# Optimization experiments

Hardware: AMD Instinct MI355X
Metric: run time of the kernel (lower is better)

Reference implementation:

```python
import jax, jax.numpy as jnp
import numpy as np

B, T, D = 4, 2048, 1024
N, H = 16, 64          # num_heads, key_dim = D // N
F = 4096               # intermediate_dim
SOFT_CAP = 50.0
EPS = 1e-6


def layer_norm(x, gamma, beta, eps=EPS):
    mean = jnp.mean(x, axis=-1, keepdims=True)
    var = jnp.var(x, axis=-1, keepdims=True)
    return (x - mean) * jax.lax.rsqrt(var + eps) * gamma + beta


def setup_inputs() -> dict:
    key = jax.random.key(0)
    ks = jax.random.split(key, 16)
    s = 0.02
    return {
        "inputs": jax.random.normal(ks[0], (B, T, D), dtype=jnp.float32),
        "ln1_gamma": jnp.ones((D,), jnp.float32),
        "ln1_beta": jnp.zeros((D,), jnp.float32),
        "wq": jax.random.normal(ks[1], (D, N, H), jnp.float32) * s,
        "bq": jnp.zeros((N, H), jnp.float32),
        "wk": jax.random.normal(ks[2], (D, N, H), jnp.float32) * s,
        "bk": jnp.zeros((N, H), jnp.float32),
        "wv": jax.random.normal(ks[3], (D, N, H), jnp.float32) * s,
        "bv": jnp.zeros((N, H), jnp.float32),
        "wo": jax.random.normal(ks[4], (N, H, D), jnp.float32) * s,
        "bo": jnp.zeros((D,), jnp.float32),
        "ln2_gamma": jnp.ones((D,), jnp.float32),
        "ln2_beta": jnp.zeros((D,), jnp.float32),
        "w1": jax.random.normal(ks[5], (D, F), jnp.float32) * s,
        "b1": jax.random.normal(ks[6], (F,), jnp.float32) * 1e-6,
        "w2": jax.random.normal(ks[7], (F, D), jnp.float32) * s,
        "b2": jax.random.normal(ks[8], (D,), jnp.float32) * 1e-6,
    }


def reference(inputs, ln1_gamma, ln1_beta, wq, bq, wk, bk, wv, bv, wo, bo,
              ln2_gamma, ln2_beta, w1, b1, w2, b2):
    # --- pre-norm attention branch ---
    x = layer_norm(inputs, ln1_gamma, ln1_beta)
    q = jnp.einsum('btd,dnh->btnh', x, wq) + bq
    k = jnp.einsum('btd,dnh->btnh', x, wk) + bk
    v = jnp.einsum('btd,dnh->btnh', x, wv) + bv
    q = q * (1.0 / jnp.sqrt(jnp.float32(H)))
    score = jnp.einsum('btnh,bsnh->bnts', q, k)          # [B,N,T,T]
    score = SOFT_CAP * jnp.tanh(score / SOFT_CAP)        # logit soft cap
    weights = jax.nn.softmax(score.astype(jnp.float32), axis=-1).astype(q.dtype)
    context = jnp.einsum('bnts,bsnh->btnh', weights, v)
    attn_out = jnp.einsum('btnh,nhd->btd', context, wo) + bo
    x_res = attn_out + inputs
    # --- pre-norm MLP branch ---
    y = layer_norm(x_res, ln2_gamma, ln2_beta)
    y = jax.nn.gelu(y @ w1 + b1, approximate=False)
    y = y @ w2 + b2
    return x_res + y
```

## Files before the change

### kernel.cpp

```cpp
#include <hip/hip_runtime.h>
#include <hip/hip_bf16.h>
#include <math.h>

typedef __attribute__((ext_vector_type(8))) short short8;
typedef __attribute__((ext_vector_type(4))) short short4v;
typedef __attribute__((ext_vector_type(4))) float f32x4;

#define GAS __attribute__((address_space(1)))
#define LAS __attribute__((address_space(3)))

__device__ __forceinline__ LAS void* to_lds(void* p) {
    return (LAS void*)(unsigned)(uintptr_t)p;
}

constexpr int Bc = 4, Tc = 2048, Dc = 1024, Nheads = 16, Hc = 64, Fc = 4096;
constexpr int Mrows = Bc * Tc;
constexpr float LNEPS = 1e-6f;

__device__ __forceinline__ float gelu_exact(float x) {
    return 0.5f * x * (1.0f + erff(x * 0.70710678118654752440f));
}

__global__ __launch_bounds__(256) void transpose_cvt(const float* __restrict__ src,
                                                     __hip_bfloat16* __restrict__ dst,
                                                     int K, int N) {
    __shared__ float tile[32][33];
    const int n0 = blockIdx.x * 32, k0 = blockIdx.y * 32;
    const int tx = threadIdx.x & 31, ty = threadIdx.x >> 5;
    #pragma unroll
    for (int i = 0; i < 32; i += 8)
        tile[ty + i][tx] = src[(size_t)(k0 + ty + i) * N + (n0 + tx)];
    __syncthreads();
    #pragma unroll
    for (int i = 0; i < 32; i += 8)
        dst[(size_t)(n0 + ty + i) * K + (k0 + tx)] = __float2bfloat16(tile[tx][ty + i]);
}

__global__ void concat_bias(const float* __restrict__ bq, const float* __restrict__ bk,
                            const float* __restrict__ bv, float* __restrict__ dst) {
    int i = blockIdx.x * 256 + threadIdx.x;
    float v = (i < 1024) ? bq[i] : (i < 2048 ? bk[i - 1024] : bv[i - 2048]);
    dst[i] = v;
}

__global__ __launch_bounds__(256) void ln_kernel(const float* __restrict__ x,
                                                 const float* __restrict__ gamma,
                                                 const float* __restrict__ beta,
                                                 __hip_bfloat16* __restrict__ out) {
    __shared__ float2 red[4];
    const int row = blockIdx.x, tid = threadIdx.x;
    const float* xr = x + (size_t)row * Dc;
    float4 v = ((const float4*)xr)[tid];
    float s  = v.x + v.y + v.z + v.w;
    float ss = v.x * v.x + v.y * v.y + v.z * v.z + v.w * v.w;
    #pragma unroll
    for (int o = 32; o; o >>= 1) { s += __shfl_down(s, o, 64); ss += __shfl_down(ss, o, 64); }
    if ((tid & 63) == 0) red[tid >> 6] = make_float2(s, ss);
    __syncthreads();
    float2 r0 = red[0], r1 = red[1], r2 = red[2], r3 = red[3];
    s  = r0.x + r1.x + r2.x + r3.x;
    ss = r0.y + r1.y + r2.y + r3.y;
    const float mean = s * (1.0f / Dc);
    const float var  = ss * (1.0f / Dc) - mean * mean;
    const float inv  = rsqrtf(var + LNEPS);
    float4 g  = ((const float4*)gamma)[tid];
    float4 bb = ((const float4*)beta)[tid];
    __hip_bfloat16* orow = out + (size_t)row * Dc + tid * 4;
    orow[0] = __float2bfloat16((v.x - mean) * inv * g.x + bb.x);
    orow[1] = __float2bfloat16((v.y - mean) * inv * g.y + bb.y);
    orow[2] = __float2bfloat16((v.z - mean) * inv * g.z + bb.z);
    orow[3] = __float2bfloat16((v.w - mean) * inv * g.w + bb.w);
}

template <int EPI, bool OUT_BF16>
__global__ __launch_bounds__(256) void gemm_kernel(
    const __hip_bfloat16* __restrict__ A, const __hip_bfloat16* __restrict__ Bt,
    const float* __restrict__ bias, const float* __restrict__ resid,
    void* __restrict__ Cout, int M, int N, int K) {
    __shared__ __align__(16) short As[128 * 32];
    __shared__ __align__(16) short Bs[128 * 32];
    const int tid = threadIdx.x;
    const int wave = tid >> 6, lane = tid & 63, quad = lane >> 4, l16 = lane & 15;
    const int m0 = blockIdx.x * 128, n0 = blockIdx.y * 128;
    const int wm = (wave >> 1) * 64, wn = (wave & 1) * 64;
    f32x4 acc[4][4] = {};

    const int srow = wave * 16 + (lane >> 2);
    const int scol = (lane & 3) * 8;
    const short* aSrc0 = (const short*)A  + (size_t)(m0 + srow) * K + scol;
    const short* aSrc1 = aSrc0 + (size_t)64 * K;
    const short* bSrc0 = (const short*)Bt + (size_t)(n0 + srow) * K + scol;
    const short* bSrc1 = bSrc0 + (size_t)64 * K;
    LAS void* ldsA0 = to_lds(&As[(wave * 16) * 32]);
    LAS void* ldsA1 = to_lds(&As[(64 + wave * 16) * 32]);
    LAS void* ldsB0 = to_lds(&Bs[(wave * 16) * 32]);
    LAS void* ldsB1 = to_lds(&Bs[(64 + wave * 16) * 32]);

    for (int k0 = 0; k0 < K; k0 += 32) {
        __builtin_amdgcn_global_load_lds((const GAS void*)(aSrc0 + k0), ldsA0, 16, 0, 0);
        __builtin_amdgcn_global_load_lds((const GAS void*)(aSrc1 + k0), ldsA1, 16, 0, 0);
        __builtin_amdgcn_global_load_lds((const GAS void*)(bSrc0 + k0), ldsB0, 16, 0, 0);
        __builtin_amdgcn_global_load_lds((const GAS void*)(bSrc1 + k0), ldsB1, 16, 0, 0);
        __syncthreads();
        short8 af[4], bfr[4];
        #pragma unroll
        for (int i = 0; i < 4; i++) af[i]  = *(const short8*)&As[(wm + i * 16 + l16) * 32 + quad * 8];
        #pragma unroll
        for (int i = 0; i < 4; i++) bfr[i] = *(const short8*)&Bs[(wn + i * 16 + l16) * 32 + quad * 8];
        #pragma unroll
        for (int i = 0; i < 4; i++)
            #pragma unroll
            for (int j = 0; j < 4; j++)
                acc[i][j] = __builtin_amdgcn_mfma_f32_16x16x32_bf16(af[i], bfr[j], acc[i][j], 0, 0, 0);
        __syncthreads();
    }
    #pragma unroll
    for (int i = 0; i < 4; i++) {
        #pragma unroll
        for (int j = 0; j < 4; j++) {
            const int col = n0 + wn + j * 16 + l16;
            const float bv = bias[col];
            #pragma unroll
            for (int r = 0; r < 4; r++) {
                const int row = m0 + wm + i * 16 + quad * 4 + r;
                float val = acc[i][j][r] + bv;
                if (EPI == 1) val = gelu_exact(val);
                if (EPI == 2) val += resid[(size_t)row * N + col];
                if (OUT_BF16)
                    ((__hip_bfloat16*)Cout)[(size_t)row * N + col] = __float2bfloat16(val);
                else
                    ((float*)Cout)[(size_t)row * N + col] = val;
            }
        }
    }
}

__global__ __launch_bounds__(256) void gemm_splitk(
    const __hip_bfloat16* __restrict__ A, const __hip_bfloat16* __restrict__ Bt,
    const float* __restrict__ bias, const float* __restrict__ resid,
    float* __restrict__ out, int M, int N, int K, int Kslice) {
    __shared__ __align__(16) short As[128 * 32];
    __shared__ __align__(16) short Bs[128 * 32];
    const int tid = threadIdx.x;
    const int wave = tid >> 6, lane = tid & 63, quad = lane >> 4, l16 = lane & 15;
    const int m0 = blockIdx.x * 128, n0 = blockIdx.y * 128;
    const int kz = blockIdx.z;
    const int wm = (wave >> 1) * 64, wn = (wave & 1) * 64;
    f32x4 acc[4][4] = {};

    const int srow = wave * 16 + (lane >> 2);
    const int scol = (lane & 3) * 8 + kz * Kslice;
    const short* aSrc0 = (const short*)A  + (size_t)(m0 + srow) * K + scol;
    const short* aSrc1 = aSrc0 + (size_t)64 * K;
    const short* bSrc0 = (const short*)Bt + (size_t)(n0 + srow) * K + scol;
    const short* bSrc1 = bSrc0 + (size_t)64 * K;
    LAS void* ldsA0 = to_lds(&As[(wave * 16) * 32]);
    LAS void* ldsA1 = to_lds(&As[(64 + wave * 16) * 32]);
    LAS void* ldsB0 = to_lds(&Bs[(wave * 16) * 32]);
    LAS void* ldsB1 = to_lds(&Bs[(64 + wave * 16) * 32]);

    for (int k0 = 0; k0 < Kslice; k0 += 32) {
        __builtin_amdgcn_global_load_lds((const GAS void*)(aSrc0 + k0), ldsA0, 16, 0, 0);
        __builtin_amdgcn_global_load_lds((const GAS void*)(aSrc1 + k0), ldsA1, 16, 0, 0);
        __builtin_amdgcn_global_load_lds((const GAS void*)(bSrc0 + k0), ldsB0, 16, 0, 0);
        __builtin_amdgcn_global_load_lds((const GAS void*)(bSrc1 + k0), ldsB1, 16, 0, 0);
        __syncthreads();
        short8 af[4], bfr[4];
        #pragma unroll
        for (int i = 0; i < 4; i++) af[i]  = *(const short8*)&As[(wm + i * 16 + l16) * 32 + quad * 8];
        #pragma unroll
        for (int i = 0; i < 4; i++) bfr[i] = *(const short8*)&Bs[(wn + i * 16 + l16) * 32 + quad * 8];
        #pragma unroll
        for (int i = 0; i < 4; i++)
            #pragma unroll
            for (int j = 0; j < 4; j++)
                acc[i][j] = __builtin_amdgcn_mfma_f32_16x16x32_bf16(af[i], bfr[j], acc[i][j], 0, 0, 0);
        __syncthreads();
    }
    #pragma unroll
    for (int i = 0; i < 4; i++) {
        #pragma unroll
        for (int j = 0; j < 4; j++) {
            const int col = n0 + wn + j * 16 + l16;
            const float bv = (kz == 0) ? bias[col] : 0.0f;
            #pragma unroll
            for (int r = 0; r < 4; r++) {
                const int row = m0 + wm + i * 16 + quad * 4 + r;
                float val = acc[i][j][r] + bv;
                if (kz == 0) val += resid[(size_t)row * N + col];
                atomicAdd(&out[(size_t)row * N + col], val);
            }
        }
    }
}

__global__ __launch_bounds__(256, 4) void flash_attn(const __hip_bfloat16* __restrict__ qkv,
                                                     __hip_bfloat16* __restrict__ ctx) {
    constexpr int NHD = 3072;
    constexpr int LQ = 72;
    constexpr int LP = 72;
    __shared__ __align__(16) short Ks[64 * LQ];
    __shared__ __align__(16) short Vt[64 * LQ];
    __shared__ __align__(16) short Ps[4 * 32 * LP];

    const int tid = threadIdx.x;
    const int wave = tid >> 6, lane = tid & 63, quad = lane >> 4, l16 = lane & 15;
    const int t0 = blockIdx.x * 128;
    const int bb = blockIdx.y >> 4, hn = blockIdx.y & 15;
    const __hip_bfloat16* Qg = qkv + ((size_t)(bb * Tc + t0)) * NHD + hn * Hc;
    const __hip_bfloat16* Kg = qkv + (size_t)bb * Tc * NHD + Dc + hn * Hc;
    const __hip_bfloat16* Vg = Kg + Dc;

    const int wm = wave * 32;
    short* Psw = Ps + wave * 32 * LP;

    short8 bq[2][2];
    #pragma unroll
    for (int kt = 0; kt < 2; ++kt)
        #pragma unroll
        for (int i = 0; i < 2; ++i)
            bq[kt][i] = *(const short8*)&Qg[(size_t)(wm + i * 16 + l16) * NHD + kt * 32 + quad * 8];

    const short4v ONES4 = {0x3F80, 0x3F80, 0x3F80, 0x3F80};
    short8 ones;
    *(short4v*)&ones = ONES4;
    *((short4v*)&ones + 1) = ONES4;

    f32x4 o_acc[2][4] = {};
    f32x4 l_mf[2]  = {};

    constexpr float C0 = 0.125f;
    constexpr float C1 = -2.60416667e-7f;
    constexpr float C2 = 6.51041667e-13f;

    for (int s0 = 0; s0 < Tc; s0 += 64) {
        __syncthreads();
        {
            const int r = tid >> 3, c = (tid & 7) * 8;
            #pragma unroll
            for (int p = 0; p < 2; ++p) {
                const int s = r + p * 32;
                *(short8*)&Ks[s * LQ + c] = *(const short8*)&Kg[(size_t)(s0 + s) * NHD + c];
                short8 vv = *(const short8*)&Vg[(size_t)(s0 + s) * NHD + c];
                #pragma unroll
                for (int j = 0; j < 8; ++j)
                    Vt[(c + j) * LQ + (s ^ c)] = ((short*)&vv)[j];
            }
        }
        __syncthreads();

        #pragma unroll
        for (int jh = 0; jh < 2; ++jh) {
            f32x4 st[2][2] = {};
            #pragma unroll
            for (int kt = 0; kt < 2; ++kt) {
                short8 ak[2];
                #pragma unroll
                for (int jj = 0; jj < 2; ++jj)
                    ak[jj] = *(const short8*)&Ks[((jh * 2 + jj) * 16 + l16) * LQ + kt * 32 + quad * 8];
                #pragma unroll
                for (int jj = 0; jj < 2; ++jj)
                    #pragma unroll
                    for (int i = 0; i < 2; ++i)
                        st[jj][i] = __builtin_amdgcn_mfma_f32_16x16x32_bf16(ak[jj], bq[kt][i], st[jj][i], 0, 0, 0);
            }
            #pragma unroll
            for (int jj = 0; jj < 2; ++jj)
                #pragma unroll
                for (int i = 0; i < 2; ++i) {
                    union { short4v v; unsigned short u[4]; } pk;
                    #pragma unroll
                    for (int r = 0; r < 4; ++r) {
                        const float sc = st[jj][i][r];
                        const float u  = sc * sc;
                        float t = sc * fmaf(fmaf(C2, u, C1), u, C0);
                        t = fminf(t, 60.0f);
                        const float p = __expf(t);
                        __hip_bfloat16 h = __float2bfloat16(p);
                        pk.u[r] = __builtin_bit_cast(unsigned short, h);
                    }
                    *(short4v*)&Psw[(i * 16 + l16) * LP + (jh * 2 + jj) * 16 + quad * 4] = pk.v;
                }
        }
        asm volatile("" ::: "memory");

        #pragma unroll
        for (int kt = 0; kt < 2; ++kt) {
            short8 ap[2], bv_[4];
            #pragma unroll
            for (int i = 0; i < 2; ++i)
                ap[i] = *(const short8*)&Psw[(i * 16 + l16) * LP + kt * 32 + quad * 8];
            #pragma unroll
            for (int ht = 0; ht < 4; ++ht) {
                const int swzV = ht * 16 + (l16 >> 3) * 8;
                bv_[ht] = *(const short8*)&Vt[(ht * 16 + l16) * LQ + ((kt * 32 + quad * 8) ^ swzV)];
            }
            #pragma unroll
            for (int i = 0; i < 2; ++i)
                l_mf[i] = __builtin_amdgcn_mfma_f32_16x16x32_bf16(ap[i], ones, l_mf[i], 0, 0, 0);
            #pragma unroll
            for (int i = 0; i < 2; ++i)
                #pragma unroll
                for (int ht = 0; ht < 4; ++ht)
                    o_acc[i][ht] = __builtin_amdgcn_mfma_f32_16x16x32_bf16(ap[i], bv_[ht], o_acc[i][ht], 0, 0, 0);
        }
        asm volatile("" ::: "memory");
    }

    #pragma unroll
    for (int i = 0; i < 2; ++i) {
        float linv[4];
        #pragma unroll
        for (int r = 0; r < 4; ++r) linv[r] = 1.0f / l_mf[i][r];
        #pragma unroll
        for (int ht = 0; ht < 4; ++ht)
            #pragma unroll
            for (int r = 0; r < 4; ++r) {
                const int row = t0 + wm + i * 16 + quad * 4 + r;
                const int col = hn * Hc + ht * 16 + l16;
                ctx[((size_t)(bb * Tc + row)) * Dc + col] =
                    __float2bfloat16(o_acc[i][ht][r] * linv[r]);
            }
    }
}

extern "C" void kernel_launch(void* const* d_in, const int* in_sizes, int n_in,
                              void* d_out, int out_size, void* d_ws, size_t ws_size,
                              hipStream_t stream) {
    const float* inputs = (const float*)d_in[0];
    const float* ln1_g  = (const float*)d_in[1];
    const float* ln1_b  = (const float*)d_in[2];
    const float* wq     = (const float*)d_in[3];
    const float* bq     = (const float*)d_in[4];
    const float* wk     = (const float*)d_in[5];
    const float* bk     = (const float*)d_in[6];
    const float* wv     = (const float*)d_in[7];
    const float* bv     = (const float*)d_in[8];
    const float* wo     = (const float*)d_in[9];
    const float* bo     = (const float*)d_in[10];
    const float* ln2_g  = (const float*)d_in[11];
    const float* ln2_b  = (const float*)d_in[12];
    const float* w1     = (const float*)d_in[13];
    const float* b1     = (const float*)d_in[14];
    const float* w2     = (const float*)d_in[15];
    const float* b2     = (const float*)d_in[16];

    char* ws = (char*)d_ws;
    auto alloc = [&](size_t bytes) {
        char* p = ws;
        ws += (bytes + 255) & ~(size_t)255;
        return p;
    };
    __hip_bfloat16* wqkv_t = (__hip_bfloat16*)alloc((size_t)3072 * 1024 * 2);
    __hip_bfloat16* wo_t   = (__hip_bfloat16*)alloc((size_t)1024 * 1024 * 2);
    __hip_bfloat16* w1_t   = (__hip_bfloat16*)alloc((size_t)4096 * 1024 * 2);
    __hip_bfloat16* w2_t   = (__hip_bfloat16*)alloc((size_t)4096 * 1024 * 2);
    float*          bqkv   = (float*)alloc(3072 * 4);
    __hip_bfloat16* xn     = (__hip_bfloat16*)alloc((size_t)Mrows * 1024 * 2);
    __hip_bfloat16* qkv    = (__hip_bfloat16*)alloc((size_t)Mrows * 3072 * 2);
    __hip_bfloat16* ctx    = (__hip_bfloat16*)alloc((size_t)Mrows * 1024 * 2);
    float*          xres   = (float*)alloc((size_t)Mrows * 1024 * 4);
    __hip_bfloat16* y1     = qkv;

    dim3 blk(256);
    transpose_cvt<<<dim3(32, 32), blk, 0, stream>>>(wq, wqkv_t, 1024, 1024);
    transpose_cvt<<<dim3(32, 32), blk, 0, stream>>>(wk, wqkv_t + 1024 * 1024, 1024, 1024);
    transpose_cvt<<<dim3(32, 32), blk, 0, stream>>>(wv, wqkv_t + 2048 * 1024, 1024, 1024);
    transpose_cvt<<<dim3(32, 32), blk, 0, stream>>>(wo, wo_t, 1024, 1024);
    transpose_cvt<<<dim3(128, 32), blk, 0, stream>>>(w1, w1_t, 1024, 4096);
    transpose_cvt<<<dim3(32, 128), blk, 0, stream>>>(w2, w2_t, 4096, 1024);
    concat_bias<<<dim3(12), blk, 0, stream>>>(bq, bk, bv, bqkv);

    ln_kernel<<<dim3(Mrows), blk, 0, stream>>>(inputs, ln1_g, ln1_b, xn);
    gemm_kernel<0, true><<<dim3(64, 24), blk, 0, stream>>>(xn, wqkv_t, bqkv, nullptr, qkv, Mrows, 3072, 1024);
    flash_attn<<<dim3(Tc / 128, Bc * Nheads), blk, 0, stream>>>(qkv, ctx);
    gemm_kernel<2, false><<<dim3(64, 8), blk, 0, stream>>>(ctx, wo_t, bo, inputs, xres, Mrows, 1024, 1024);
    ln_kernel<<<dim3(Mrows), blk, 0, stream>>>(xres, ln2_g, ln2_b, xn);
    gemm_kernel<1, true><<<dim3(64, 32), blk, 0, stream>>>(xn, w1_t, b1, nullptr, y1, Mrows, 4096, 1024);
    hipMemsetAsync(d_out, 0, (size_t)out_size * sizeof(float), stream);
    gemm_splitk<<<dim3(64, 8, 2), blk, 0, stream>>>(y1, w2_t, b2, xres, (float*)d_out, Mrows, 1024, 4096, 2048);
}
```

Baseline: 650.1 us.

## Pre-transpose V globally for attention and drop split-K for the final GEMM

Adds a separate kernel that transposes V from the packed QKV buffer into a per-head [H,T] layout, so flash attention can load V tiles into LDS with vector stores instead of scalar transposing stores and XOR swizzle. It also replaces the split-K atomic GEMM plus memset for the second MLP projection with the regular tiled GEMM using the residual epilogue. The cost is an extra launch and an extra pass over V through global memory. The final GEMM now has only 512 blocks, so it may fill the device less well.

After: 608.0 us. 1.07x faster.

```diff
diff --git a/kernel.cpp b/kernel.cpp
--- a/kernel.cpp
+++ b/kernel.cpp
@@ -34,6 +34,23 @@
     #pragma unroll
     for (int i = 0; i < 32; i += 8)
         dst[(size_t)(n0 + ty + i) * K + (k0 + tx)] = __float2bfloat16(tile[tx][ty + i]);
+}
+
+__global__ __launch_bounds__(256) void transpose_v(const __hip_bfloat16* __restrict__ qkv,
+                                                   __hip_bfloat16* __restrict__ vT) {
+    __shared__ short tile[32][33];
+    const int t0 = blockIdx.x * 32, h0 = blockIdx.y * 32, bn = blockIdx.z;
+    const int b = bn >> 4, n = bn & 15;
+    const short* src = (const short*)qkv + (size_t)b * Tc * 3072 + 2048 + n * 64;
+    short* dst = (short*)vT + (size_t)bn * 64 * Tc;
+    const int tx = threadIdx.x & 31, ty = threadIdx.x >> 5;
+    #pragma unroll
+    for (int i = 0; i < 32; i += 8)
+        tile[ty + i][tx] = src[(size_t)(t0 + ty + i) * 3072 + h0 + tx];
+    __syncthreads();
+    #pragma unroll
+    for (int i = 0; i < 32; i += 8)
+        dst[(size_t)(h0 + ty + i) * Tc + t0 + tx] = tile[tx][ty + i];
 }
 
 __global__ void concat_bias(const float* __restrict__ bq, const float* __restrict__ bk,
@@ -135,66 +152,8 @@
     }
 }
 
-__global__ __launch_bounds__(256) void gemm_splitk(
-    const __hip_bfloat16* __restrict__ A, const __hip_bfloat16* __restrict__ Bt,
-    const float* __restrict__ bias, const float* __restrict__ resid,
-    float* __restrict__ out, int M, int N, int K, int Kslice) {
-    __shared__ __align__(16) short As[128 * 32];
-    __shared__ __align__(16) short Bs[128 * 32];
-    const int tid = threadIdx.x;
-    const int wave = tid >> 6, lane = tid & 63, quad = lane >> 4, l16 = lane & 15;
-    const int m0 = blockIdx.x * 128, n0 = blockIdx.y * 128;
-    const int kz = blockIdx.z;
-    const int wm = (wave >> 1) * 64, wn = (wave & 1) * 64;
-    f32x4 acc[4][4] = {};
-
-    const int srow = wave * 16 + (lane >> 2);
-    const int scol = (lane & 3) * 8 + kz * Kslice;
-    const short* aSrc0 = (const short*)A  + (size_t)(m0 + srow) * K + scol;
-    const short* aSrc1 = aSrc0 + (size_t)64 * K;
-    const short* bSrc0 = (const short*)Bt + (size_t)(n0 + srow) * K + scol;
-    const short* bSrc1 = bSrc0 + (size_t)64 * K;
-    LAS void* ldsA0 = to_lds(&As[(wave * 16) * 32]);
-    LAS void* ldsA1 = to_lds(&As[(64 + wave * 16) * 32]);
-    LAS void* ldsB0 = to_lds(&Bs[(wave * 16) * 32]);
-    LAS void* ldsB1 = to_lds(&Bs[(64 + wave * 16) * 32]);
-
-    for (int k0 = 0; k0 < Kslice; k0 += 32) {
-        __builtin_amdgcn_global_load_lds((const GAS void*)(aSrc0 + k0), ldsA0, 16, 0, 0);
-        __builtin_amdgcn_global_load_lds((const GAS void*)(aSrc1 + k0), ldsA1, 16, 0, 0);
-        __builtin_amdgcn_global_load_lds((const GAS void*)(bSrc0 + k0), ldsB0, 16, 0, 0);
-        __builtin_amdgcn_global_load_lds((const GAS void*)(bSrc1 + k0), ldsB1, 16, 0, 0);
-        __syncthreads();
-        short8 af[4], bfr[4];
-        #pragma unroll
-        for (int i = 0; i < 4; i++) af[i]  = *(const short8*)&As[(wm + i * 16 + l16) * 32 + quad * 8];
-        #pragma unroll
-        for (int i = 0; i < 4; i++) bfr[i] = *(const short8*)&Bs[(wn + i * 16 + l16) * 32 + quad * 8];
-        #pragma unroll
-        for (int i = 0; i < 4; i++)
-            #pragma unroll
-            for (int j = 0; j < 4; j++)
-                acc[i][j] = __builtin_amdgcn_mfma_f32_16x16x32_bf16(af[i], bfr[j], acc[i][j], 0, 0, 0);
-        __syncthreads();
-    }
-    #pragma unroll
-    for (int i = 0; i < 4; i++) {
-        #pragma unroll
-        for (int j = 0; j < 4; j++) {
-            const int col = n0 + wn + j * 16 + l16;
-            const float bv = (kz == 0) ? bias[col] : 0.0f;
-            #pragma unroll
-            for (int r = 0; r < 4; r++) {
-                const int row = m0 + wm + i * 16 + quad * 4 + r;
-                float val = acc[i][j][r] + bv;
-                if (kz == 0) val += resid[(size_t)row * N + col];
-                atomicAdd(&out[(size_t)row * N + col], val);
-            }
-        }
-    }
-}
-
 __global__ __launch_bounds__(256, 4) void flash_attn(const __hip_bfloat16* __restrict__ qkv,
+                                                     const __hip_bfloat16* __restrict__ vT,
                                                      __hip_bfloat16* __restrict__ ctx) {
     constexpr int NHD = 3072;
     constexpr int LQ = 72;
@@ -206,10 +165,11 @@
     const int tid = threadIdx.x;
     const int wave = tid >> 6, lane = tid & 63, quad = lane >> 4, l16 = lane & 15;
     const int t0 = blockIdx.x * 128;
-    const int bb = blockIdx.y >> 4, hn = blockIdx.y & 15;
-    const __hip_bfloat16* Qg = qkv + ((size_t)(bb * Tc + t0)) * NHD + hn * Hc;
-    const __hip_bfloat16* Kg = qkv + (size_t)bb * Tc * NHD + Dc + hn * Hc;
-    const __hip_bfloat16* Vg = Kg + Dc;
+    const int bn = blockIdx.y;
+    const int bb = bn >> 4, hn = bn & 15;
+    const __hip_bfloat16* Qg  = qkv + ((size_t)(bb * Tc + t0)) * NHD + hn * Hc;
+    const __hip_bfloat16* Kg  = qkv + (size_t)bb * Tc * NHD + Dc + hn * Hc;
+    const __hip_bfloat16* vTg = vT + (size_t)bn * 64 * Tc;
 
     const int wm = wave * 32;
     short* Psw = Ps + wave * 32 * LP;
@@ -241,10 +201,7 @@
             for (int p = 0; p < 2; ++p) {
                 const int s = r + p * 32;
                 *(short8*)&Ks[s * LQ + c] = *(const short8*)&Kg[(size_t)(s0 + s) * NHD + c];
-                short8 vv = *(const short8*)&Vg[(size_t)(s0 + s) * NHD + c];
-                #pragma unroll
-                for (int j = 0; j < 8; ++j)
-                    Vt[(c + j) * LQ + (s ^ c)] = ((short*)&vv)[j];
+                *(short8*)&Vt[s * LQ + c] = *(const short8*)&vTg[(size_t)s * Tc + s0 + c];
             }
         }
         __syncthreads();
@@ -291,10 +248,8 @@
             for (int i = 0; i < 2; ++i)
                 ap[i] = *(const short8*)&Psw[(i * 16 + l16) * LP + kt * 32 + quad * 8];
             #pragma unroll
-            for (int ht = 0; ht < 4; ++ht) {
-                const int swzV = ht * 16 + (l16 >> 3) * 8;
-                bv_[ht] = *(const short8*)&Vt[(ht * 16 + l16) * LQ + ((kt * 32 + quad * 8) ^ swzV)];
-            }
+            for (int ht = 0; ht < 4; ++ht)
+                bv_[ht] = *(const short8*)&Vt[(ht * 16 + l16) * LQ + kt * 32 + quad * 8];
             #pragma unroll
             for (int i = 0; i < 2; ++i)
                 l_mf[i] = __builtin_amdgcn_mfma_f32_16x16x32_bf16(ap[i], ones, l_mf[i], 0, 0, 0);
@@ -358,6 +313,7 @@
     float*          bqkv   = (float*)alloc(3072 * 4);
     __hip_bfloat16* xn     = (__hip_bfloat16*)alloc((size_t)Mrows * 1024 * 2);
     __hip_bfloat16* qkv    = (__hip_bfloat16*)alloc((size_t)Mrows * 3072 * 2);
+    __hip_bfloat16* vTr    = (__hip_bfloat16*)alloc((size_t)64 * 64 * Tc * 2);
     __hip_bfloat16* ctx    = (__hip_bfloat16*)alloc((size_t)Mrows * 1024 * 2);
     float*          xres   = (float*)alloc((size_t)Mrows * 1024 * 4);
     __hip_bfloat16* y1     = qkv;
@@ -373,10 +329,10 @@
 
     ln_kernel<<<dim3(Mrows), blk, 0, stream>>>(inputs, ln1_g, ln1_b, xn);
     gemm_kernel<0, true><<<dim3(64, 24), blk, 0, stream>>>(xn, wqkv_t, bqkv, nullptr, qkv, Mrows, 3072, 1024);
-    flash_attn<<<dim3(Tc / 128, Bc * Nheads), blk, 0, stream>>>(qkv, ctx);
+    transpose_v<<<dim3(64, 2, 64), blk, 0, stream>>>(qkv, vTr);
+    flash_attn<<<dim3(Tc / 128, Bc * Nheads), blk, 0, stream>>>(qkv, vTr, ctx);
     gemm_kernel<2, false><<<dim3(64, 8), blk, 0, stream>>>(ctx, wo_t, bo, inputs, xres, Mrows, 1024, 1024);
     ln_kernel<<<dim3(Mrows), blk, 0, stream>>>(xres, ln2_g, ln2_b, xn);
     gemm_kernel<1, true><<<dim3(64, 32), blk, 0, stream>>>(xn, w1_t, b1, nullptr, y1, Mrows, 4096, 1024);
-    hipMemsetAsync(d_out, 0, (size_t)out_size * sizeof(float), stream);
-    gemm_splitk<<<dim3(64, 8, 2), blk, 0, stream>>>(y1, w2_t, b2, xres, (float*)d_out, Mrows, 1024, 4096, 2048);
-}
+    gemm_kernel<2, false><<<dim3(64, 8), blk, 0, stream>>>(y1, w2_t, b2, xres, (float*)d_out, Mrows, 1024, 4096);
+}
```
